# Kernel tuning notes

Measured on AMD Instinct MI355X. Metric: run time of the kernel, lower is better.

The kernel has to match this reference:

```python
import jax, jax.numpy as jnp
import numpy as np

NU, NV, NF = 100000, 50000, 5000
D = 64
S, EUV = 5, 500000
EUF, EVF, EFU, EFV = 1000000, 500000, 1000000, 500000


def _spmm(rows, cols, vals, x, n_out):
    # COO sparse @ dense: out[r] += v * x[c]
    return jax.ops.segment_sum(vals[:, None] * x[cols], rows, num_segments=n_out)


def setup_inputs() -> dict:
    key = jax.random.key(0)
    ks = iter(jax.random.split(key, 32))
    f32 = jnp.float32
    inp = {
        'x_u': jax.random.normal(next(ks), (NU, D), f32),
        'x_v': jax.random.normal(next(ks), (NV, D), f32),
        'x_f': jax.random.normal(next(ks), (NF, D), f32),
    }
    for w in ['W_u_uv', 'W_v_uv', 'W_f2u', 'W_f2v', 'W_u2f', 'W_v2f']:
        inp[w] = jax.random.normal(next(ks), (D, D), f32) * (1.0 / np.sqrt(D))
    def edges(name, shape, n_row, n_col):
        inp[name + '_rows'] = jax.random.randint(next(ks), shape, 0, n_row, jnp.int32)
        inp[name + '_cols'] = jax.random.randint(next(ks), shape, 0, n_col, jnp.int32)
        inp[name + '_vals'] = jax.random.uniform(next(ks), shape, f32)
    edges('uv', (S, EUV), NU, NV)
    edges('vu', (S, EUV), NV, NU)
    edges('uf', (EUF,), NU, NF)
    edges('vf', (EVF,), NV, NF)
    edges('fu', (EFU,), NF, NU)
    edges('fv', (EFV,), NF, NV)
    return inp


def reference(x_u, x_v, x_f, W_u_uv, W_v_uv, W_f2u, W_f2v, W_u2f, W_v2f,
              uv_rows, uv_cols, uv_vals, vu_rows, vu_cols, vu_vals,
              uf_rows, uf_cols, uf_vals, vf_rows, vf_cols, vf_vals,
              fu_rows, fu_cols, fu_vals, fv_rows, fv_cols, fv_vals):
    nu, nv, nf = x_u.shape[0], x_v.shape[0], x_f.shape[0]
    # dense feature transforms (dropout=0 -> identity)
    u2f = x_u @ W_u2f
    v2f = x_v @ W_v2f
    f2u = x_f @ W_f2u
    f2v = x_f @ W_f2v
    tmp_u = x_u @ W_u_uv
    tmp_v = x_v @ W_v_uv
    # sum over rating supports == one segment_sum over flattened edges
    msg_u = _spmm(uv_rows.reshape(-1), uv_cols.reshape(-1), uv_vals.reshape(-1), tmp_v, nu)
    msg_v = _spmm(vu_rows.reshape(-1), vu_cols.reshape(-1), vu_vals.reshape(-1), tmp_u, nv)
    msg_u = msg_u + _spmm(uf_rows, uf_cols, uf_vals, f2u, nu)
    msg_v = msg_v + _spmm(vf_rows, vf_cols, vf_vals, f2v, nv)
    msg_f = _spmm(fu_rows, fu_cols, fu_vals, u2f, nf) + _spmm(fv_rows, fv_cols, fv_vals, v2f, nf)
    return jax.nn.relu(msg_u), jax.nn.relu(msg_v), jax.nn.relu(msg_f)
```

## Files before the change

kernel.cpp:

```cpp
#include <hip/hip_runtime.h>


#define TDIM 64
#define EPB  4096
#define STCAP 10240

struct Rel {
    const int* rows; const int* cols; const float* vals;
    int n, chunk0, boff, shift, srcflag, eoff, coladd;
};
struct RelPack { Rel r[6]; };

struct TPack {
    const float* X[3]; const float* W1[3]; const float* W2[3];
    unsigned short* Y1[3]; unsigned short* Y2[3];
    int N[3]; int c0[3];
};

struct FSPack {
    int c0A[3], cntA[3], offA[3];
    int c0B[3], cntB[3], offB[3];
};

struct GatherPack {
    const unsigned* srcA[3]; const unsigned* srcB[3];
    int n0, n1;
};

__device__ __forceinline__ unsigned short f2bf(float f) {
    union { float f; unsigned u; } c; c.f = f;
    unsigned r = c.u + 0x7FFFu + ((c.u >> 16) & 1u);
    return (unsigned short)(r >> 16);
}
__device__ __forceinline__ float bflo(unsigned x) { return __uint_as_float(x << 16); }
__device__ __forceinline__ float bfhi(unsigned x) { return __uint_as_float(x & 0xFFFF0000u); }
__device__ __forceinline__ float pval(unsigned p) {
    return __uint_as_float((p & 0x7FFFu) << 16);
}

__global__ __launch_bounds__(256) void transform_fused_kernel(TPack T)
{
    __shared__ float xsT[64 * 68];
    __shared__ float w1s[64 * 64];
    __shared__ float w2s[64 * 64];

    int t = 0;
    if ((int)blockIdx.x >= T.c0[1]) t = 1;
    if ((int)blockIdx.x >= T.c0[2]) t = 2;
    const float* __restrict__ X  = T.X[t];
    const float* __restrict__ W1 = T.W1[t];
    const float* __restrict__ W2 = T.W2[t];
    unsigned short* __restrict__ Y1 = T.Y1[t];
    unsigned short* __restrict__ Y2 = T.Y2[t];
    const int N    = T.N[t];
    const int row0 = (blockIdx.x - T.c0[t]) * 64;
    const int tid  = threadIdx.x;

    for (int i = tid * 4; i < 4096; i += 256 * 4) {
        *(float4*)&w1s[i] = *(const float4*)&W1[i];
        *(float4*)&w2s[i] = *(const float4*)&W2[i];
    }
    {
        const int r  = tid >> 2;
        const int c0 = (tid & 3) * 16;
        const int gr = row0 + r;
        #pragma unroll
        for (int cc = 0; cc < 16; cc += 4) {
            const int c = c0 + cc;
            float4 v = make_float4(0.f, 0.f, 0.f, 0.f);
            if (gr < N) v = *(const float4*)&X[(size_t)gr * TDIM + c];
            xsT[(c + 0) * 68 + r] = v.x;
            xsT[(c + 1) * 68 + r] = v.y;
            xsT[(c + 2) * 68 + r] = v.z;
            xsT[(c + 3) * 68 + r] = v.w;
        }
    }
    __syncthreads();

    const int tx = tid & 15;
    const int ty = tid >> 4;
    float a1[4][4] = {{0.f}}, a2[4][4] = {{0.f}};

    #pragma unroll 8
    for (int k = 0; k < 64; ++k) {
        const float4 xv = *(const float4*)&xsT[k * 68 + ty * 4];
        const float4 w1 = *(const float4*)&w1s[k * 64 + tx * 4];
        const float4 w2 = *(const float4*)&w2s[k * 64 + tx * 4];
        const float xr[4] = {xv.x, xv.y, xv.z, xv.w};
        const float c1[4] = {w1.x, w1.y, w1.z, w1.w};
        const float c2[4] = {w2.x, w2.y, w2.z, w2.w};
        #pragma unroll
        for (int r = 0; r < 4; ++r)
            #pragma unroll
            for (int c = 0; c < 4; ++c) {
                a1[r][c] = fmaf(xr[r], c1[c], a1[r][c]);
                a2[r][c] = fmaf(xr[r], c2[c], a2[r][c]);
            }
    }
    #pragma unroll
    for (int r = 0; r < 4; ++r) {
        const int gr = row0 + ty * 4 + r;
        if (gr < N) {
            ushort4 o1, o2;
            o1.x = f2bf(a1[r][0]); o1.y = f2bf(a1[r][1]);
            o1.z = f2bf(a1[r][2]); o1.w = f2bf(a1[r][3]);
            o2.x = f2bf(a2[r][0]); o2.y = f2bf(a2[r][1]);
            o2.z = f2bf(a2[r][2]); o2.w = f2bf(a2[r][3]);
            ((ushort4*)Y1)[(size_t)gr * 16 + tx] = o1;
            ((ushort4*)Y2)[(size_t)gr * 16 + tx] = o2;
        }
    }
}

__device__ __forceinline__ int find_rel(const RelPack& P, int chunk) {
    int ri = 0;
    if (chunk >= P.r[1].chunk0) ri = 1;
    if (chunk >= P.r[2].chunk0) ri = 2;
    if (chunk >= P.r[3].chunk0) ri = 3;
    if (chunk >= P.r[4].chunk0) ri = 4;
    if (chunk >= P.r[5].chunk0) ri = 5;
    return ri;
}

__global__ __launch_bounds__(512) void bucketize_cm_kernel(
    RelPack P, unsigned* __restrict__ pay, unsigned char* __restrict__ binb,
    unsigned short* __restrict__ localStart, int* __restrict__ bucketTotal,
    int NB)
{
    __shared__ int cnt[1536];
    __shared__ int sh[512];
    __shared__ unsigned stage_pay[EPB];
    __shared__ unsigned char stage_bin[EPB];

    const int tid   = threadIdx.x;
    const int chunk = blockIdx.x;
    for (int t = tid; t < NB; t += 512) cnt[t] = 0;
    __syncthreads();

    const int ri = find_rel(P, chunk);
    const Rel M = P.r[ri];
    const int i0    = (chunk - M.chunk0) * EPB;
    const int rbase = M.eoff + i0;
    const int count = min(EPB, M.n - i0);

    const int mask = (1 << M.shift) - 1;
    const unsigned sf = (unsigned)M.srcflag;

    int      m_[EPB / 512];
    unsigned x_[EPB / 512];
    #pragma unroll
    for (int k = 0; k < EPB / 512; ++k) {
        const int i = i0 + tid + k * 512;
        m_[k] = -1;
        if (i < M.n) {
            const int row = M.rows[i];
            const int b   = M.boff + (row >> M.shift);
            m_[k] = (b << 8) | (row & mask);
            const unsigned colp = (unsigned)M.cols[i] + (unsigned)M.coladd;
            x_[k] = (colp << 15) | ((unsigned)f2bf(M.vals[i]) & 0x7FFFu);
            atomicAdd(&cnt[b], 1);
        }
    }
    __syncthreads();

    int myv[3]; int lsum = 0;
    #pragma unroll
    for (int j = 0; j < 3; ++j) {
        const int idx = tid * 3 + j;
        myv[j] = (idx < NB) ? cnt[idx] : 0;
        lsum += myv[j];
    }
    sh[tid] = lsum;
    __syncthreads();
    for (int off = 1; off < 512; off <<= 1) {
        const int x = (tid >= off) ? sh[tid - off] : 0;
        __syncthreads();
        sh[tid] += x;
        __syncthreads();
    }
    int prefix = tid ? sh[tid - 1] : 0;
    const size_t lb = (size_t)chunk * (NB + 1);
    #pragma unroll
    for (int j = 0; j < 3; ++j) {
        const int idx = tid * 3 + j;
        if (idx < NB) {
            localStart[lb + idx] = (unsigned short)prefix;
            if (myv[j]) atomicAdd(&bucketTotal[idx], myv[j]);
            cnt[idx] = prefix;
        } else if (idx == NB) {
            localStart[lb + NB] = (unsigned short)prefix;
        }
        prefix += myv[j];
    }
    __syncthreads();

    #pragma unroll
    for (int k = 0; k < EPB / 512; ++k) {
        if (m_[k] >= 0) {
            const int b   = m_[k] >> 8;
            const int pos = atomicAdd(&cnt[b], 1);
            stage_pay[pos] = x_[k];
            stage_bin[pos] = (unsigned char)(((m_[k] & 255) << 1) | sf);
        }
    }
    __syncthreads();

    #pragma unroll
    for (int k = 0; k < EPB / 512; ++k) {
        const int j = tid + k * 512;
        if (j < count) pay[rbase + j] = stage_pay[j];
    }
    {
        const int nfull = count >> 2;
        unsigned* bout = (unsigned*)(binb + rbase);
        const unsigned* bsrc = (const unsigned*)stage_bin;
        for (int j = tid; j < nfull; j += 512) bout[j] = bsrc[j];
        if (tid < (count & 3)) binb[rbase + nfull * 4 + tid] = stage_bin[nfull * 4 + tid];
    }
}

__global__ __launch_bounds__(256) void bscan_transpose_kernel(
    const int* __restrict__ bucketTotal, int* __restrict__ bbase, int NB,
    const unsigned short* __restrict__ src, unsigned short* __restrict__ dst,
    int rows, int cols)
{
    __shared__ int shb[256];
    __shared__ int carry;
    __shared__ unsigned short tile[32][33];

    const int t = threadIdx.x;

    if (blockIdx.x == 0 && blockIdx.y == 0) {
        if (t == 0) carry = 0;
        __syncthreads();
        for (int b0 = 0; b0 < NB; b0 += 256) {
            const int idx = b0 + t;
            const int c = (idx < NB) ? bucketTotal[idx] : 0;
            shb[t] = c;
            __syncthreads();
            for (int off = 1; off < 256; off <<= 1) {
                const int x = (t >= off) ? shb[t - off] : 0;
                __syncthreads();
                shb[t] += x;
                __syncthreads();
            }
            const int cbase = carry;
            if (idx < NB) bbase[idx] = cbase + shb[t] - c;
            __syncthreads();
            if (t == 0) carry = cbase + shb[255];
            __syncthreads();
        }
        if (t == 0) bbase[NB] = carry;
        __syncthreads();
    }

    const int c0 = blockIdx.x * 32;
    const int r0 = blockIdx.y * 32;
    const int tx = t & 31;
    const int ty = t >> 5;
    #pragma unroll
    for (int k = 0; k < 32; k += 8) {
        const int r = r0 + ty + k, c = c0 + tx;
        if (r < rows && c < cols) tile[ty + k][tx] = src[(size_t)r * cols + c];
    }
    __syncthreads();
    #pragma unroll
    for (int k = 0; k < 32; k += 8) {
        const int c = c0 + ty + k, r = r0 + tx;
        if (c < cols && r < rows) dst[(size_t)c * rows + r] = tile[tx][ty + k];
    }
}

__global__ __launch_bounds__(512) void finesort_kernel(
    const unsigned* __restrict__ pay, const unsigned char* __restrict__ binb,
    const unsigned short* __restrict__ TL, const int* __restrict__ bbase,
    FSPack F, int* __restrict__ p2, unsigned* __restrict__ arena,
    int nbU, int nbV, int NU, int NV, int NF, int NB, int ntot_rows,
    int nchunksTot)
{
    __shared__ int cnt[512];
    __shared__ int sh[512];
    __shared__ int runS[1024], runE[1024];
    __shared__ unsigned stage[STCAP];

    const int b   = blockIdx.x;
    const int tid = threadIdx.x;

    int t, lb, rowbase;
    if (b < nbU)              { t = 0; lb = b;              rowbase = 0; }
    else if (b < nbU + nbV)   { t = 1; lb = b - nbU;        rowbase = NU; }
    else                      { t = 2; lb = b - nbU - nbV;  rowbase = NU + NV; }
    const int shift     = (t == 2) ? 5 : 7;
    const int Ntype     = (t == 0) ? NU : (t == 1) ? NV : NF;
    const int row_start = lb << shift;
    const int nrows     = min(1 << shift, Ntype - row_start);
    const int nbins     = (1 << shift) * 2;
    const int grow0     = rowbase + row_start;

    const int nA = F.cntA[t], nB_ = F.cntB[t];
    const int nRuns = nA + nB_;

    const unsigned short* __restrict__ TLb  = TL + (size_t)b * nchunksTot;
    const unsigned short* __restrict__ TLb1 = TL + (size_t)(b + 1) * nchunksTot;
    for (int i = tid; i < nRuns; i += 512) {
        int ci, base;
        if (i < nA) { ci = F.c0A[t] + i;        base = F.offA[t] + i * EPB; }
        else        { int k = i - nA;
                      ci = F.c0B[t] + k;        base = F.offB[t] + k * EPB; }
        runS[i] = base + (int)TLb[ci];
        runE[i] = base + (int)TLb1[ci];
    }
    if (tid < nbins) cnt[tid] = 0;
    __syncthreads();

    const int s = bbase[b];
    const int e = bbase[b + 1];
    const bool staged = (e - s) <= STCAP;
    const int grp = tid >> 2;
    const int gl  = tid & 3;

    for (int ridx = grp; ridx < nRuns; ridx += 128) {
        const int rs = runS[ridx], re = runE[ridx];
        for (int j = rs + gl; j < re; j += 4) {
            atomicAdd(&cnt[binb[j]], 1);
        }
    }
    __syncthreads();

    const int v = (tid < nbins) ? cnt[tid] : 0;
    sh[tid] = v;
    __syncthreads();
    for (int off = 1; off < 512; off <<= 1) {
        const int x = (tid >= off) ? sh[tid - off] : 0;
        __syncthreads();
        sh[tid] += x;
        __syncthreads();
    }
    const int excl = sh[tid] - v;
    if (tid < nbins) cnt[tid] = staged ? excl : (s + excl);
    if (tid < nrows * 2) p2[2 * grow0 + tid] = s + excl;
    if (b == NB - 1 && tid == 0) p2[2 * ntot_rows] = e;
    __syncthreads();

    if (staged) {
        for (int ridx = grp; ridx < nRuns; ridx += 128) {
            const int rs = runS[ridx], re = runE[ridx];
            for (int j = rs + gl; j < re; j += 4) {
                const int pos = atomicAdd(&cnt[binb[j]], 1);
                stage[pos] = pay[j];
            }
        }
        __syncthreads();
        const int seglen = e - s;
        for (int j = tid; j < seglen; j += 512) arena[s + j] = stage[j];
    } else {
        for (int ridx = grp; ridx < nRuns; ridx += 128) {
            const int rs = runS[ridx], re = runE[ridx];
            for (int j = rs + gl; j < re; j += 4) {
                const int pos = atomicAdd(&cnt[binb[j]], 1);
                arena[pos] = pay[j];
            }
        }
    }
}

__device__ __forceinline__ void accum_seg(
    const unsigned* __restrict__ src, const unsigned* __restrict__ arena,
    const int s, const int e, const int g, const int li4,
    float (&acc)[8])
{
    if (s >= e) return;
    const int nb = (e - s + 7) >> 3;
    const unsigned* __restrict__ srcp = src + li4;

    unsigned x0[4], x1[4], x2[4], x3[4];
    float w0, w1, w2, w3;

    auto issue = [&](int j, unsigned* x, float& w) {
        const int idx = j + g;
        const bool ok = idx < e;
        const unsigned cv = arena[ok ? idx : s];
        w = ok ? pval(cv) : 0.f;
        const uint4 xv = *(const uint4*)&srcp[(cv >> 15) * 32u];
        x[0] = xv.x; x[1] = xv.y; x[2] = xv.z; x[3] = xv.w;
    };
    auto fmab = [&](const unsigned* x, float w) {
        #pragma unroll
        for (int q = 0; q < 4; ++q) {
            acc[2 * q]     = fmaf(w, bflo(x[q]), acc[2 * q]);
            acc[2 * q + 1] = fmaf(w, bfhi(x[q]), acc[2 * q + 1]);
        }
    };

    issue(s,      x0, w0);
    issue(s + 8,  x1, w1);
    issue(s + 16, x2, w2);
    issue(s + 24, x3, w3);
    __builtin_amdgcn_sched_barrier(0);

    int k = 0;
    for (;;) {
        fmab(x0, w0);
        if (k + 4 < nb) issue(s + (k + 4) * 8, x0, w0);
        __builtin_amdgcn_sched_barrier(0);
        if (++k >= nb) break;
        fmab(x1, w1);
        if (k + 4 < nb) issue(s + (k + 4) * 8, x1, w1);
        __builtin_amdgcn_sched_barrier(0);
        if (++k >= nb) break;
        fmab(x2, w2);
        if (k + 4 < nb) issue(s + (k + 4) * 8, x2, w2);
        __builtin_amdgcn_sched_barrier(0);
        if (++k >= nb) break;
        fmab(x3, w3);
        if (k + 4 < nb) issue(s + (k + 4) * 8, x3, w3);
        __builtin_amdgcn_sched_barrier(0);
        if (++k >= nb) break;
    }
}

__global__ __launch_bounds__(256) void gather_all_kernel(
    const int* __restrict__ p2, const unsigned* __restrict__ arena,
    GatherPack G, float* __restrict__ out, int nrow_total)
{
    const int gid  = (blockIdx.x * 256 + threadIdx.x) >> 6;
    const int lane = threadIdx.x & 63;
    const int g    = lane >> 3;
    const int li   = lane & 7;
    const int li4  = li * 4;
    if (gid >= nrow_total) return;
    const int wid = nrow_total - 1 - gid;

    int seg = 0;
    if (wid >= G.n1)      seg = 2;
    else if (wid >= G.n0) seg = 1;
    seg = __builtin_amdgcn_readfirstlane(seg);

    const int pa = __builtin_amdgcn_readfirstlane(p2[2 * wid]);
    const int pe = __builtin_amdgcn_readfirstlane(p2[2 * wid + 2]);

    float acc[8];
    #pragma unroll
    for (int k = 0; k < 8; ++k) acc[k] = 0.f;

    if (seg < 2) {
        accum_seg(G.srcA[seg], arena, pa, pe, g, li4, acc);
    } else {
        const int pm = __builtin_amdgcn_readfirstlane(p2[2 * wid + 1]);
        accum_seg(G.srcA[2], arena, pa, pm, g, li4, acc);
        accum_seg(G.srcB[2], arena, pm, pe, g, li4, acc);
    }

    #pragma unroll
    for (int k = 0; k < 8; ++k) {
        acc[k] += __shfl_xor(acc[k], 8, 64);
        acc[k] += __shfl_xor(acc[k], 16, 64);
        acc[k] += __shfl_xor(acc[k], 32, 64);
    }

    if (g == 0) {
        float4 o0, o1;
        o0.x = fmaxf(acc[0], 0.f); o0.y = fmaxf(acc[1], 0.f);
        o0.z = fmaxf(acc[2], 0.f); o0.w = fmaxf(acc[3], 0.f);
        o1.x = fmaxf(acc[4], 0.f); o1.y = fmaxf(acc[5], 0.f);
        o1.z = fmaxf(acc[6], 0.f); o1.w = fmaxf(acc[7], 0.f);
        float4* dst = (float4*)(out + (size_t)wid * 64 + li * 8);
        dst[0] = o0;
        dst[1] = o1;
    }
}

extern "C" void kernel_launch(void* const* d_in, const int* in_sizes, int n_in,
                              void* d_out, int out_size, void* d_ws, size_t ws_size,
                              hipStream_t stream)
{
    const float* x_u    = (const float*)d_in[0];
    const float* x_v    = (const float*)d_in[1];
    const float* x_f    = (const float*)d_in[2];
    const float* W_u_uv = (const float*)d_in[3];
    const float* W_v_uv = (const float*)d_in[4];
    const float* W_f2u  = (const float*)d_in[5];
    const float* W_f2v  = (const float*)d_in[6];
    const float* W_u2f  = (const float*)d_in[7];
    const float* W_v2f  = (const float*)d_in[8];

    const int* rows_[6] = {(const int*)d_in[9],  (const int*)d_in[12],
                           (const int*)d_in[15], (const int*)d_in[18],
                           (const int*)d_in[21], (const int*)d_in[24]};
    const int* cols_[6] = {(const int*)d_in[10], (const int*)d_in[13],
                           (const int*)d_in[16], (const int*)d_in[19],
                           (const int*)d_in[22], (const int*)d_in[25]};
    const float* vals_[6] = {(const float*)d_in[11], (const float*)d_in[14],
                             (const float*)d_in[17], (const float*)d_in[20],
                             (const float*)d_in[23], (const float*)d_in[26]};

    const int NU = in_sizes[0] / TDIM;
    const int NV = in_sizes[1] / TDIM;
    const int NF = in_sizes[2] / TDIM;
    const int E_[6] = {in_sizes[9], in_sizes[12], in_sizes[15],
                       in_sizes[18], in_sizes[21], in_sizes[24]};

    const int nbU = (NU + 127) >> 7;
    const int nbV = (NV + 127) >> 7;
    const int nbF = (NF + 31) >> 5;
    const int NB  = nbU + nbV + nbF;
    const int ntot_rows = NU + NV + NF;

    const int boff_[6]   = {0, nbU, 0, nbU, nbU + nbV, nbU + nbV};
    const int shift_[6]  = {7, 7, 7, 7, 5, 5};
    const int sflag_[6]  = {0, 0, 1, 1, 0, 1};
    const int coladd_[6] = {0, 0, NV, NU, 0, 0};

    size_t etot = 0;
    int eoff_[6];
    for (int r = 0; r < 6; ++r) { eoff_[r] = (int)etot; etot += (size_t)E_[r]; }

    RelPack P;
    int nchunks = 0;
    int relchunks[6];
    for (int r = 0; r < 6; ++r) {
        P.r[r].rows = rows_[r]; P.r[r].cols = cols_[r]; P.r[r].vals = vals_[r];
        P.r[r].n = E_[r]; P.r[r].chunk0 = nchunks;
        P.r[r].boff = boff_[r]; P.r[r].shift = shift_[r]; P.r[r].srcflag = sflag_[r];
        P.r[r].eoff = eoff_[r]; P.r[r].coladd = coladd_[r];
        relchunks[r] = (E_[r] + EPB - 1) / EPB;
        nchunks += relchunks[r];
    }

    char* wsb = (char*)d_ws;
    size_t o = 0;
    auto alloc = [&](size_t bytes) {
        char* p = wsb + o;
        o = (o + bytes + 15) & ~(size_t)15;
        return p;
    };
    unsigned short* utab = (unsigned short*)alloc(((size_t)NV + NF) * TDIM * 2);
    unsigned short* vtab = (unsigned short*)alloc(((size_t)NU + NF) * TDIM * 2);
    unsigned short* u2f  = (unsigned short*)alloc((size_t)NU * TDIM * 2);
    unsigned short* v2f  = (unsigned short*)alloc((size_t)NV * TDIM * 2);
    unsigned short* tmp_v = utab;
    unsigned short* f2u   = utab + (size_t)NV * TDIM;
    unsigned short* tmp_u = vtab;
    unsigned short* f2v   = vtab + (size_t)NU * TDIM;
    unsigned short* localStart16 = (unsigned short*)alloc((size_t)nchunks * (NB + 1) * 2);
    unsigned short* TL16         = (unsigned short*)alloc((size_t)(NB + 1) * nchunks * 2);
    int* bucketTotal = (int*)alloc((size_t)NB * 4);
    int* bbase       = (int*)alloc((size_t)(NB + 1) * 4);
    int* p2          = (int*)alloc((size_t)(2 * ntot_rows + 1) * 4);
    unsigned* pay        = (unsigned*)alloc(etot * 4);
    unsigned char* binb  = (unsigned char*)alloc(etot);
    unsigned* arena      = (unsigned*)alloc(etot * 4);
    (void)ws_size;

    TPack T;
    T.X[0] = x_u; T.W1[0] = W_u_uv; T.W2[0] = W_u2f; T.Y1[0] = tmp_u; T.Y2[0] = u2f; T.N[0] = NU;
    T.X[1] = x_v; T.W1[1] = W_v_uv; T.W2[1] = W_v2f; T.Y1[1] = tmp_v; T.Y2[1] = v2f; T.N[1] = NV;
    T.X[2] = x_f; T.W1[2] = W_f2u;  T.W2[2] = W_f2v; T.Y1[2] = f2u;  T.Y2[2] = f2v; T.N[2] = NF;
    T.c0[0] = 0;
    T.c0[1] = (NU + 63) / 64;
    T.c0[2] = T.c0[1] + (NV + 63) / 64;
    const int tchunks = T.c0[2] + (NF + 63) / 64;
    transform_fused_kernel<<<tchunks, 256, 0, stream>>>(T);

    hipMemsetAsync(bucketTotal, 0, (size_t)NB * sizeof(int), stream);
    bucketize_cm_kernel<<<nchunks, 512, 0, stream>>>(P, pay, binb, localStart16, bucketTotal, NB);
    {
        dim3 tgrid((NB + 1 + 31) / 32, (nchunks + 31) / 32);
        bscan_transpose_kernel<<<tgrid, 256, 0, stream>>>(
            bucketTotal, bbase, NB, localStart16, TL16, nchunks, NB + 1);
    }

    FSPack F;
    const int Arel[3] = {0, 1, 4}, Brel[3] = {2, 3, 5};
    for (int t = 0; t < 3; ++t) {
        F.c0A[t] = P.r[Arel[t]].chunk0; F.cntA[t] = relchunks[Arel[t]]; F.offA[t] = eoff_[Arel[t]];
        F.c0B[t] = P.r[Brel[t]].chunk0; F.cntB[t] = relchunks[Brel[t]]; F.offB[t] = eoff_[Brel[t]];
    }
    finesort_kernel<<<NB, 512, 0, stream>>>(
        pay, binb, TL16, bbase, F, p2, arena, nbU, nbV, NU, NV, NF, NB, ntot_rows, nchunks);

    GatherPack G;
    G.srcA[0] = (const unsigned*)utab;  G.srcB[0] = (const unsigned*)utab;
    G.srcA[1] = (const unsigned*)vtab;  G.srcB[1] = (const unsigned*)vtab;
    G.srcA[2] = (const unsigned*)u2f;   G.srcB[2] = (const unsigned*)v2f;
    G.n0 = NU; G.n1 = NU + NV;

    gather_all_kernel<<<(ntot_rows + 3) / 4, 256, 0, stream>>>(
        p2, arena, G, (float*)d_out, ntot_rows);
}
```

Measured before the change: 500.8 us.

## Fuse fine sort with per-row gather, keeping sorted segments in shared memory

Merges the fine-sort and gather kernels so each bucket block sorts its edges into shared memory and immediately accumulates its rows from there. This removes the global arena write and re-read, the p2 row-pointer array, and the bucket-total atomics and global scan, since segment extents now come from a local scan. Oversized buckets fall back to a global buffer claimed through an atomic cursor. The catch is that the gather now runs inside 512-thread blocks that hold large shared memory, which can lower occupancy and parallelism for the latency-bound gather.

After: 428.4 us. -14.5%, faster.

```diff
diff --git a/kernel.cpp b/kernel.cpp
--- a/kernel.cpp
+++ b/kernel.cpp
@@ -20,11 +20,6 @@
 struct FSPack {
     int c0A[3], cntA[3], offA[3];
     int c0B[3], cntB[3], offB[3];
-};
-
-struct GatherPack {
-    const unsigned* srcA[3]; const unsigned* srcB[3];
-    int n0, n1;
 };
 
 __device__ __forceinline__ unsigned short f2bf(float f) {
@@ -124,8 +119,7 @@
 
 __global__ __launch_bounds__(512) void bucketize_cm_kernel(
     RelPack P, unsigned* __restrict__ pay, unsigned char* __restrict__ binb,
-    unsigned short* __restrict__ localStart, int* __restrict__ bucketTotal,
-    int NB)
+    unsigned short* __restrict__ localStart, int NB)
 {
     __shared__ int cnt[1536];
     __shared__ int sh[512];
@@ -185,7 +179,6 @@
         const int idx = tid * 3 + j;
         if (idx < NB) {
             localStart[lb + idx] = (unsigned short)prefix;
-            if (myv[j]) atomicAdd(&bucketTotal[idx], myv[j]);
             cnt[idx] = prefix;
         } else if (idx == NB) {
             localStart[lb + NB] = (unsigned short)prefix;
@@ -219,45 +212,15 @@
     }
 }
 
-__global__ __launch_bounds__(256) void bscan_transpose_kernel(
-    const int* __restrict__ bucketTotal, int* __restrict__ bbase, int NB,
+__global__ __launch_bounds__(256) void transpose16_kernel(
     const unsigned short* __restrict__ src, unsigned short* __restrict__ dst,
     int rows, int cols)
 {
-    __shared__ int shb[256];
-    __shared__ int carry;
     __shared__ unsigned short tile[32][33];
-
-    const int t = threadIdx.x;
-
-    if (blockIdx.x == 0 && blockIdx.y == 0) {
-        if (t == 0) carry = 0;
-        __syncthreads();
-        for (int b0 = 0; b0 < NB; b0 += 256) {
-            const int idx = b0 + t;
-            const int c = (idx < NB) ? bucketTotal[idx] : 0;
-            shb[t] = c;
-            __syncthreads();
-            for (int off = 1; off < 256; off <<= 1) {
-                const int x = (t >= off) ? shb[t - off] : 0;
-                __syncthreads();
-                shb[t] += x;
-                __syncthreads();
-            }
-            const int cbase = carry;
-            if (idx < NB) bbase[idx] = cbase + shb[t] - c;
-            __syncthreads();
-            if (t == 0) carry = cbase + shb[255];
-            __syncthreads();
-        }
-        if (t == 0) bbase[NB] = carry;
-        __syncthreads();
-    }
-
     const int c0 = blockIdx.x * 32;
     const int r0 = blockIdx.y * 32;
-    const int tx = t & 31;
-    const int ty = t >> 5;
+    const int tx = threadIdx.x & 31;
+    const int ty = threadIdx.x >> 5;
     #pragma unroll
     for (int k = 0; k < 32; k += 8) {
         const int r = r0 + ty + k, c = c0 + tx;
@@ -271,101 +234,8 @@
     }
 }
 
-__global__ __launch_bounds__(512) void finesort_kernel(
-    const unsigned* __restrict__ pay, const unsigned char* __restrict__ binb,
-    const unsigned short* __restrict__ TL, const int* __restrict__ bbase,
-    FSPack F, int* __restrict__ p2, unsigned* __restrict__ arena,
-    int nbU, int nbV, int NU, int NV, int NF, int NB, int ntot_rows,
-    int nchunksTot)
-{
-    __shared__ int cnt[512];
-    __shared__ int sh[512];
-    __shared__ int runS[1024], runE[1024];
-    __shared__ unsigned stage[STCAP];
-
-    const int b   = blockIdx.x;
-    const int tid = threadIdx.x;
-
-    int t, lb, rowbase;
-    if (b < nbU)              { t = 0; lb = b;              rowbase = 0; }
-    else if (b < nbU + nbV)   { t = 1; lb = b - nbU;        rowbase = NU; }
-    else                      { t = 2; lb = b - nbU - nbV;  rowbase = NU + NV; }
-    const int shift     = (t == 2) ? 5 : 7;
-    const int Ntype     = (t == 0) ? NU : (t == 1) ? NV : NF;
-    const int row_start = lb << shift;
-    const int nrows     = min(1 << shift, Ntype - row_start);
-    const int nbins     = (1 << shift) * 2;
-    const int grow0     = rowbase + row_start;
-
-    const int nA = F.cntA[t], nB_ = F.cntB[t];
-    const int nRuns = nA + nB_;
-
-    const unsigned short* __restrict__ TLb  = TL + (size_t)b * nchunksTot;
-    const unsigned short* __restrict__ TLb1 = TL + (size_t)(b + 1) * nchunksTot;
-    for (int i = tid; i < nRuns; i += 512) {
-        int ci, base;
-        if (i < nA) { ci = F.c0A[t] + i;        base = F.offA[t] + i * EPB; }
-        else        { int k = i - nA;
-                      ci = F.c0B[t] + k;        base = F.offB[t] + k * EPB; }
-        runS[i] = base + (int)TLb[ci];
-        runE[i] = base + (int)TLb1[ci];
-    }
-    if (tid < nbins) cnt[tid] = 0;
-    __syncthreads();
-
-    const int s = bbase[b];
-    const int e = bbase[b + 1];
-    const bool staged = (e - s) <= STCAP;
-    const int grp = tid >> 2;
-    const int gl  = tid & 3;
-
-    for (int ridx = grp; ridx < nRuns; ridx += 128) {
-        const int rs = runS[ridx], re = runE[ridx];
-        for (int j = rs + gl; j < re; j += 4) {
-            atomicAdd(&cnt[binb[j]], 1);
-        }
-    }
-    __syncthreads();
-
-    const int v = (tid < nbins) ? cnt[tid] : 0;
-    sh[tid] = v;
-    __syncthreads();
-    for (int off = 1; off < 512; off <<= 1) {
-        const int x = (tid >= off) ? sh[tid - off] : 0;
-        __syncthreads();
-        sh[tid] += x;
-        __syncthreads();
-    }
-    const int excl = sh[tid] - v;
-    if (tid < nbins) cnt[tid] = staged ? excl : (s + excl);
-    if (tid < nrows * 2) p2[2 * grow0 + tid] = s + excl;
-    if (b == NB - 1 && tid == 0) p2[2 * ntot_rows] = e;
-    __syncthreads();
-
-    if (staged) {
-        for (int ridx = grp; ridx < nRuns; ridx += 128) {
-            const int rs = runS[ridx], re = runE[ridx];
-            for (int j = rs + gl; j < re; j += 4) {
-                const int pos = atomicAdd(&cnt[binb[j]], 1);
-                stage[pos] = pay[j];
-            }
-        }
-        __syncthreads();
-        const int seglen = e - s;
-        for (int j = tid; j < seglen; j += 512) arena[s + j] = stage[j];
-    } else {
-        for (int ridx = grp; ridx < nRuns; ridx += 128) {
-            const int rs = runS[ridx], re = runE[ridx];
-            for (int j = rs + gl; j < re; j += 4) {
-                const int pos = atomicAdd(&cnt[binb[j]], 1);
-                arena[pos] = pay[j];
-            }
-        }
-    }
-}
-
 __device__ __forceinline__ void accum_seg(
-    const unsigned* __restrict__ src, const unsigned* __restrict__ arena,
+    const unsigned* __restrict__ src, const unsigned* seg,
     const int s, const int e, const int g, const int li4,
     float (&acc)[8])
 {
@@ -379,7 +249,7 @@
     auto issue = [&](int j, unsigned* x, float& w) {
         const int idx = j + g;
         const bool ok = idx < e;
-        const unsigned cv = arena[ok ? idx : s];
+        const unsigned cv = seg[ok ? idx : s];
         w = ok ? pval(cv) : 0.f;
         const uint4 xv = *(const uint4*)&srcp[(cv >> 15) * 32u];
         x[0] = xv.x; x[1] = xv.y; x[2] = xv.z; x[3] = xv.w;
@@ -419,54 +289,144 @@
     }
 }
 
-__global__ __launch_bounds__(256) void gather_all_kernel(
-    const int* __restrict__ p2, const unsigned* __restrict__ arena,
-    GatherPack G, float* __restrict__ out, int nrow_total)
+__global__ __launch_bounds__(512) void finesort_gather_kernel(
+    const unsigned* __restrict__ pay, const unsigned char* __restrict__ binb,
+    const unsigned short* __restrict__ TL, FSPack F,
+    const unsigned* __restrict__ srcU, const unsigned* __restrict__ srcV,
+    const unsigned* __restrict__ srcFA, const unsigned* __restrict__ srcFB,
+    unsigned* __restrict__ fbuf, int* __restrict__ fbCursor,
+    float* __restrict__ out,
+    int nbU, int nbV, int NU, int NV, int NF, int NB, int nchunksTot)
 {
-    const int gid  = (blockIdx.x * 256 + threadIdx.x) >> 6;
-    const int lane = threadIdx.x & 63;
+    __shared__ int cnt[256];
+    __shared__ int sh[512];
+    __shared__ int rowptr[257];
+    __shared__ int runS[1024];
+    __shared__ unsigned short runL[1024];
+    __shared__ unsigned stage[STCAP];
+    __shared__ int fbOff;
+
+    const int b   = NB - 1 - (int)blockIdx.x;
+    const int tid = threadIdx.x;
+
+    int t, lb, rowbase;
+    if (b < nbU)              { t = 0; lb = b;              rowbase = 0; }
+    else if (b < nbU + nbV)   { t = 1; lb = b - nbU;        rowbase = NU; }
+    else                      { t = 2; lb = b - nbU - nbV;  rowbase = NU + NV; }
+    const int shift     = (t == 2) ? 5 : 7;
+    const int Ntype     = (t == 0) ? NU : (t == 1) ? NV : NF;
+    const int row_start = lb << shift;
+    const int nrows     = min(1 << shift, Ntype - row_start);
+    const int nbins     = (1 << shift) * 2;
+    const int grow0     = rowbase + row_start;
+
+    const int nA = F.cntA[t], nB_ = F.cntB[t];
+    const int nRuns = nA + nB_;
+
+    const unsigned short* __restrict__ TLb  = TL + (size_t)b * nchunksTot;
+    const unsigned short* __restrict__ TLb1 = TL + (size_t)(b + 1) * nchunksTot;
+    for (int i = tid; i < nRuns; i += 512) {
+        int ci, base;
+        if (i < nA) { ci = F.c0A[t] + i;        base = F.offA[t] + i * EPB; }
+        else        { int k = i - nA;
+                      ci = F.c0B[t] + k;        base = F.offB[t] + k * EPB; }
+        const int s0 = (int)TLb[ci];
+        runS[i] = base + s0;
+        runL[i] = (unsigned short)((int)TLb1[ci] - s0);
+    }
+    if (tid < nbins) cnt[tid] = 0;
+    __syncthreads();
+
+    const int grp = tid >> 2;
+    const int gl  = tid & 3;
+
+    for (int ridx = grp; ridx < nRuns; ridx += 128) {
+        const int rs = runS[ridx], re = rs + (int)runL[ridx];
+        for (int j = rs + gl; j < re; j += 4) {
+            atomicAdd(&cnt[binb[j]], 1);
+        }
+    }
+    __syncthreads();
+
+    const int v = (tid < nbins) ? cnt[tid] : 0;
+    sh[tid] = v;
+    __syncthreads();
+    for (int off = 1; off < 512; off <<= 1) {
+        const int x = (tid >= off) ? sh[tid - off] : 0;
+        __syncthreads();
+        sh[tid] += x;
+        __syncthreads();
+    }
+    const int tot = sh[511];
+    const bool staged = tot <= STCAP;
+    const int excl = sh[tid] - v;
+    if (tid < nbins) { cnt[tid] = excl; rowptr[tid] = excl; }
+    if (tid == 0) {
+        rowptr[nbins] = tot;
+        if (!staged) fbOff = atomicAdd(fbCursor, tot);
+    }
+    __syncthreads();
+
+    if (staged) {
+        for (int ridx = grp; ridx < nRuns; ridx += 128) {
+            const int rs = runS[ridx], re = rs + (int)runL[ridx];
+            for (int j = rs + gl; j < re; j += 4) {
+                const int pos = atomicAdd(&cnt[binb[j]], 1);
+                stage[pos] = pay[j];
+            }
+        }
+    } else {
+        unsigned* fb = fbuf + fbOff;
+        for (int ridx = grp; ridx < nRuns; ridx += 128) {
+            const int rs = runS[ridx], re = rs + (int)runL[ridx];
+            for (int j = rs + gl; j < re; j += 4) {
+                const int pos = atomicAdd(&cnt[binb[j]], 1);
+                fb[pos] = pay[j];
+            }
+        }
+    }
+    __syncthreads();
+
+    const unsigned* seg = staged ? (const unsigned*)stage
+                                 : (const unsigned*)(fbuf + fbOff);
+    const int wave = tid >> 6;
+    const int lane = tid & 63;
     const int g    = lane >> 3;
     const int li   = lane & 7;
     const int li4  = li * 4;
-    if (gid >= nrow_total) return;
-    const int wid = nrow_total - 1 - gid;
-
-    int seg = 0;
-    if (wid >= G.n1)      seg = 2;
-    else if (wid >= G.n0) seg = 1;
-    seg = __builtin_amdgcn_readfirstlane(seg);
-
-    const int pa = __builtin_amdgcn_readfirstlane(p2[2 * wid]);
-    const int pe = __builtin_amdgcn_readfirstlane(p2[2 * wid + 2]);
-
-    float acc[8];
-    #pragma unroll
-    for (int k = 0; k < 8; ++k) acc[k] = 0.f;
-
-    if (seg < 2) {
-        accum_seg(G.srcA[seg], arena, pa, pe, g, li4, acc);
-    } else {
-        const int pm = __builtin_amdgcn_readfirstlane(p2[2 * wid + 1]);
-        accum_seg(G.srcA[2], arena, pa, pm, g, li4, acc);
-        accum_seg(G.srcB[2], arena, pm, pe, g, li4, acc);
-    }
-
-    #pragma unroll
-    for (int k = 0; k < 8; ++k) {
-        acc[k] += __shfl_xor(acc[k], 8, 64);
-        acc[k] += __shfl_xor(acc[k], 16, 64);
-        acc[k] += __shfl_xor(acc[k], 32, 64);
-    }
-
-    if (g == 0) {
-        float4 o0, o1;
-        o0.x = fmaxf(acc[0], 0.f); o0.y = fmaxf(acc[1], 0.f);
-        o0.z = fmaxf(acc[2], 0.f); o0.w = fmaxf(acc[3], 0.f);
-        o1.x = fmaxf(acc[4], 0.f); o1.y = fmaxf(acc[5], 0.f);
-        o1.z = fmaxf(acc[6], 0.f); o1.w = fmaxf(acc[7], 0.f);
-        float4* dst = (float4*)(out + (size_t)wid * 64 + li * 8);
-        dst[0] = o0;
-        dst[1] = o1;
+    const unsigned* srcUni = (t == 0) ? srcU : srcV;
+
+    for (int r = wave; r < nrows; r += 8) {
+        const int sA = rowptr[2 * r];
+        const int eR = rowptr[2 * r + 2];
+        float acc[8];
+        #pragma unroll
+        for (int k = 0; k < 8; ++k) acc[k] = 0.f;
+
+        if (t < 2) {
+            accum_seg(srcUni, seg, sA, eR, g, li4, acc);
+        } else {
+            const int sB = rowptr[2 * r + 1];
+            accum_seg(srcFA, seg, sA, sB, g, li4, acc);
+            accum_seg(srcFB, seg, sB, eR, g, li4, acc);
+        }
+
+        #pragma unroll
+        for (int k = 0; k < 8; ++k) {
+            acc[k] += __shfl_xor(acc[k], 8, 64);
+            acc[k] += __shfl_xor(acc[k], 16, 64);
+            acc[k] += __shfl_xor(acc[k], 32, 64);
+        }
+        if (g == 0) {
+            float4 o0, o1;
+            o0.x = fmaxf(acc[0], 0.f); o0.y = fmaxf(acc[1], 0.f);
+            o0.z = fmaxf(acc[2], 0.f); o0.w = fmaxf(acc[3], 0.f);
+            o1.x = fmaxf(acc[4], 0.f); o1.y = fmaxf(acc[5], 0.f);
+            o1.z = fmaxf(acc[6], 0.f); o1.w = fmaxf(acc[7], 0.f);
+            float4* dst = (float4*)(out + (size_t)(grow0 + r) * 64 + li * 8);
+            dst[0] = o0;
+            dst[1] = o1;
+        }
     }
 }
 
@@ -505,6 +465,7 @@
     const int nbF = (NF + 31) >> 5;
     const int NB  = nbU + nbV + nbF;
     const int ntot_rows = NU + NV + NF;
+    (void)ntot_rows;
 
     const int boff_[6]   = {0, nbU, 0, nbU, nbU + nbV, nbU + nbV};
     const int shift_[6]  = {7, 7, 7, 7, 5, 5};
@@ -544,12 +505,10 @@
     unsigned short* f2v   = vtab + (size_t)NU * TDIM;
     unsigned short* localStart16 = (unsigned short*)alloc((size_t)nchunks * (NB + 1) * 2);
     unsigned short* TL16         = (unsigned short*)alloc((size_t)(NB + 1) * nchunks * 2);
-    int* bucketTotal = (int*)alloc((size_t)NB * 4);
-    int* bbase       = (int*)alloc((size_t)(NB + 1) * 4);
-    int* p2          = (int*)alloc((size_t)(2 * ntot_rows + 1) * 4);
     unsigned* pay        = (unsigned*)alloc(etot * 4);
     unsigned char* binb  = (unsigned char*)alloc(etot);
-    unsigned* arena      = (unsigned*)alloc(etot * 4);
+    unsigned* fbuf       = (unsigned*)alloc(etot * 4);
+    int* fbCursor        = (int*)alloc(16);
     (void)ws_size;
 
     TPack T;
@@ -562,12 +521,11 @@
     const int tchunks = T.c0[2] + (NF + 63) / 64;
     transform_fused_kernel<<<tchunks, 256, 0, stream>>>(T);
 
-    hipMemsetAsync(bucketTotal, 0, (size_t)NB * sizeof(int), stream);
-    bucketize_cm_kernel<<<nchunks, 512, 0, stream>>>(P, pay, binb, localStart16, bucketTotal, NB);
+    hipMemsetAsync(fbCursor, 0, sizeof(int), stream);
+    bucketize_cm_kernel<<<nchunks, 512, 0, stream>>>(P, pay, binb, localStart16, NB);
     {
         dim3 tgrid((NB + 1 + 31) / 32, (nchunks + 31) / 32);
-        bscan_transpose_kernel<<<tgrid, 256, 0, stream>>>(
-            bucketTotal, bbase, NB, localStart16, TL16, nchunks, NB + 1);
+        transpose16_kernel<<<tgrid, 256, 0, stream>>>(localStart16, TL16, nchunks, NB + 1);
     }
 
     FSPack F;
@@ -576,15 +534,11 @@
         F.c0A[t] = P.r[Arel[t]].chunk0; F.cntA[t] = relchunks[Arel[t]]; F.offA[t] = eoff_[Arel[t]];
         F.c0B[t] = P.r[Brel[t]].chunk0; F.cntB[t] = relchunks[Brel[t]]; F.offB[t] = eoff_[Brel[t]];
     }
-    finesort_kernel<<<NB, 512, 0, stream>>>(
-        pay, binb, TL16, bbase, F, p2, arena, nbU, nbV, NU, NV, NF, NB, ntot_rows, nchunks);
-
-    GatherPack G;
-    G.srcA[0] = (const unsigned*)utab;  G.srcB[0] = (const unsigned*)utab;
-    G.srcA[1] = (const unsigned*)vtab;  G.srcB[1] = (const unsigned*)vtab;
-    G.srcA[2] = (const unsigned*)u2f;   G.srcB[2] = (const unsigned*)v2f;
-    G.n0 = NU; G.n1 = NU + NV;
-
-    gather_all_kernel<<<(ntot_rows + 3) / 4, 256, 0, stream>>>(
-        p2, arena, G, (float*)d_out, ntot_rows);
-}
+
+    finesort_gather_kernel<<<NB, 512, 0, stream>>>(
+        pay, binb, TL16, F,
+        (const unsigned*)utab, (const unsigned*)vtab,
+        (const unsigned*)u2f,  (const unsigned*)v2f,
+        fbuf, fbCursor, (float*)d_out,
+        nbU, nbV, NU, NV, NF, NB, nchunks);
+}
```
